# Performance work log

Hardware: AMD Instinct MI355X
Metric: run time of the kernel (lower is better)

## Reference

```python
import jax, jax.numpy as jnp
import numpy as np

N_NODES = 10000
N_EDGES = 160000
HIDDEN = 512
N_LAYERS = 5


def setup_inputs() -> dict:
    key = jax.random.key(0)
    ks = jax.random.split(key, 12)
    return {
        "feat": jax.random.normal(ks[0], (N_NODES, HIDDEN), dtype=jnp.float32),
        "adj_row": jax.random.randint(ks[1], (N_EDGES,), 0, N_NODES, dtype=jnp.int32),
        "adj_col": jax.random.randint(ks[2], (N_EDGES,), 0, N_NODES, dtype=jnp.int32),
        "adj_val": jax.random.uniform(ks[3], (N_EDGES,), dtype=jnp.float32),
        "Wg": jax.random.normal(ks[4], (N_LAYERS, HIDDEN, HIDDEN), dtype=jnp.float32) * 0.02,
        "bg": jnp.zeros((N_LAYERS, HIDDEN), dtype=jnp.float32),
        "vw1": jax.random.normal(ks[5], (HIDDEN, HIDDEN), dtype=jnp.float32) * 0.02,
        "vb1": jnp.zeros((HIDDEN,), dtype=jnp.float32),
        "vw2": jax.random.normal(ks[6], (HIDDEN, 1), dtype=jnp.float32) * 0.02,
        "vb2": jnp.zeros((1,), dtype=jnp.float32),
    }


def _spmm(adj_row, adj_col, adj_val, x, n):
    # out[r] = sum_e adj_val[e] * x[adj_col[e]] for edges with adj_row[e] == r
    gathered = adj_val[:, None] * x[adj_col]  # [E, H]
    return jax.ops.segment_sum(gathered, adj_row, num_segments=n)


def reference(feat, adj_row, adj_col, adj_val, Wg, bg, vw1, vb1, vw2, vb2):
    n = feat.shape[0]
    x = feat
    for i in range(N_LAYERS):  # 5 structurally identical GraphConv layers
        h = x @ Wg[i]                                 # dense GEMM [N,H]
        agg = _spmm(adj_row, adj_col, adj_val, h, n)  # sparse aggregation
        x = jax.nn.relu(agg + bg[i])                  # bias + ReLU (dropout = eval identity)
    h = jax.nn.relu(x @ vw1 + vb1)
    return jax.nn.sigmoid(h @ vw2 + vb2)  # [N, 1]
```

## Files before the change

### kernel.cpp

```cpp
#include <hip/hip_runtime.h>

#define H 512
#define NNODES 10000
#define NEDGES 160000
#define NLAYERS 5

typedef __attribute__((ext_vector_type(8))) short short8;
typedef __attribute__((ext_vector_type(4))) float floatx4;

__device__ inline unsigned short f2bf(float v) {
    union { float f; unsigned int u; } x; x.f = v;
    unsigned int r = (x.u + 0x7fffu + ((x.u >> 16) & 1u)) >> 16;
    return (unsigned short)r;
}
__device__ inline float bf2f(unsigned short u) {
    union { unsigned int u; float f; } x; x.u = ((unsigned int)u) << 16; return x.f;
}
__device__ inline void gl_lds16(const void* g, void* l) {
    __builtin_amdgcn_global_load_lds((const __attribute__((address_space(1))) void*)g,
                                     (__attribute__((address_space(3))) void*)l, 16, 0, 0);
}

__global__ void zero_int(int* __restrict__ p, int n) {
    int i = blockIdx.x * blockDim.x + threadIdx.x;
    if (i < n) p[i] = 0;
}

__global__ void cvt_f32_bf16(const float* __restrict__ in, unsigned short* __restrict__ out, int n4) {
    int i = blockIdx.x * blockDim.x + threadIdx.x;
    if (i < n4) {
        float4 v = ((const float4*)in)[i];
        ushort4 o;
        o.x = f2bf(v.x); o.y = f2bf(v.y); o.z = f2bf(v.z); o.w = f2bf(v.w);
        ((ushort4*)out)[i] = o;
    }
}

__global__ void transpose_cvt6(const float* __restrict__ Wg, const float* __restrict__ vw1,
                               unsigned short* __restrict__ Wt) {
    __shared__ float tile[32][33];
    const int z = blockIdx.z;
    const float* in = (z < NLAYERS) ? (Wg + (size_t)z * H * H) : vw1;
    unsigned short* out = Wt + (size_t)z * H * H;
    const int bx = blockIdx.x * 32;
    const int by = blockIdx.y * 32;
    const int tx = threadIdx.x, ty = threadIdx.y;
    for (int i = ty; i < 32; i += 8)
        tile[i][tx] = in[(size_t)(by + i) * H + bx + tx];
    __syncthreads();
    for (int i = ty; i < 32; i += 8)
        out[(size_t)(bx + i) * H + by + tx] = f2bf(tile[tx][i]);
}

__global__ void edge_hist(const int* __restrict__ rows, int* __restrict__ counts, int n) {
    int i = blockIdx.x * blockDim.x + threadIdx.x;
    if (i < n) atomicAdd(&counts[rows[i]], 1);
}

__global__ __launch_bounds__(1024)
void scan_rows_pad(const int* __restrict__ counts, int* __restrict__ row_ptr, int n) {
    __shared__ int sums[1024];
    const int t = threadIdx.x;
    const int base = t * 16;
    int local[16];
    int s = 0;
#pragma unroll
    for (int i = 0; i < 16; ++i) {
        int idx = base + i;
        int v = (idx < n) ? ((counts[idx] + 7) & ~7) : 0;
        local[i] = s;
        s += v;
    }
    sums[t] = s;
    __syncthreads();
    for (int off = 1; off < 1024; off <<= 1) {
        int v = (t >= off) ? sums[t - off] : 0;
        __syncthreads();
        sums[t] += v;
        __syncthreads();
    }
    const int prefix = (t == 0) ? 0 : sums[t - 1];
#pragma unroll
    for (int i = 0; i < 16; ++i) {
        int idx = base + i;
        if (idx < n) row_ptr[idx] = prefix + local[i];
    }
    if (t == 0) row_ptr[n] = sums[1023];
}

__global__ void edge_scatter(const int* __restrict__ rows, const int* __restrict__ colsin,
                             const float* __restrict__ valsin, const int* __restrict__ row_ptr,
                             int* __restrict__ fill, int* __restrict__ colsout,
                             float* __restrict__ valsout, int n) {
    int i = blockIdx.x * blockDim.x + threadIdx.x;
    if (i < n) {
        int r = rows[i];
        int pos = row_ptr[r] + atomicAdd(&fill[r], 1);
        colsout[pos] = colsin[i];
        valsout[pos] = valsin[i];
    }
}

__device__ __forceinline__ void gemm_tile_body(
    const unsigned short* __restrict__ A, const unsigned short* __restrict__ Bt,
    unsigned short* __restrict__ C, const float* __restrict__ bias,
    int has_bias_relu, int M, int tileM, int tileN,
    unsigned short* lsA, unsigned short* lsB) {
    const int t = threadIdx.x;
    const int lane = t & 63;
    const int wave = t >> 6;
    const int wm = wave >> 1, wn = wave & 1;
    const int quad = lane >> 4, r16 = lane & 15;

    floatx4 acc[4][2] = {};

    const unsigned short* ap[4];
#pragma unroll
    for (int q = 0; q < 4; ++q) {
        const int c = t + 256 * q;
        const int row = c >> 3;
        int g = tileM + row; if (g >= M) g = M - 1;
        ap[q] = A + (size_t)g * 512 + (((c & 7) ^ (row & 7)) * 8);
    }
    const unsigned short* bp[2];
#pragma unroll
    for (int q = 0; q < 2; ++q) {
        const int c = t + 256 * q;
        const int row = c >> 3;
        bp[q] = Bt + (size_t)(tileN + row) * 512 + (((c & 7) ^ (row & 7)) * 8);
    }

    for (int k0 = 0; k0 < 512; k0 += 64) {
        gl_lds16(ap[0] + k0, lsA + (size_t)t * 8);
        gl_lds16(ap[1] + k0, lsA + (size_t)(t + 256) * 8);
        gl_lds16(ap[2] + k0, lsA + (size_t)(t + 512) * 8);
        gl_lds16(ap[3] + k0, lsA + (size_t)(t + 768) * 8);
        gl_lds16(bp[0] + k0, lsB + (size_t)t * 8);
        gl_lds16(bp[1] + k0, lsB + (size_t)(t + 256) * 8);
        __syncthreads();

        short8 af[4][2], bfr[2][2];
#pragma unroll
        for (int i = 0; i < 4; ++i) {
            const int row = wm * 64 + i * 16 + r16;
#pragma unroll
            for (int kk = 0; kk < 2; ++kk) {
                const int kcw = kk * 4 + quad;
                af[i][kk] = *(const short8*)&lsA[(size_t)(row * 8 + (kcw ^ (row & 7))) * 8];
            }
        }
#pragma unroll
        for (int j = 0; j < 2; ++j) {
            const int row = wn * 32 + j * 16 + r16;
#pragma unroll
            for (int kk = 0; kk < 2; ++kk) {
                const int kcw = kk * 4 + quad;
                bfr[j][kk] = *(const short8*)&lsB[(size_t)(row * 8 + (kcw ^ (row & 7))) * 8];
            }
        }
#pragma unroll
        for (int kk = 0; kk < 2; ++kk)
#pragma unroll
            for (int i = 0; i < 4; ++i)
#pragma unroll
                for (int j = 0; j < 2; ++j)
                    acc[i][j] = __builtin_amdgcn_mfma_f32_16x16x32_bf16(af[i][kk], bfr[j][kk], acc[i][j], 0, 0, 0);
        __syncthreads();
    }

#pragma unroll
    for (int i = 0; i < 4; ++i) {
#pragma unroll
        for (int j = 0; j < 2; ++j) {
            const int col = tileN + wn * 32 + j * 16 + r16;
#pragma unroll
            for (int reg = 0; reg < 4; ++reg) {
                const int row = tileM + wm * 64 + i * 16 + quad * 4 + reg;
                if (row < M) {
                    float v = acc[i][j][reg];
                    if (has_bias_relu) { v += bias[col]; v = fmaxf(v, 0.f); }
                    C[(size_t)row * 512 + col] = f2bf(v);
                }
            }
        }
    }
}

__global__ __launch_bounds__(256)
void gemm_bf16_xcd(const unsigned short* __restrict__ A, const unsigned short* __restrict__ Bt,
                   unsigned short* __restrict__ C, const float* __restrict__ bias,
                   int has_bias_relu, int M) {
    __shared__ __align__(16) unsigned short lsA[128 * 64];
    __shared__ __align__(16) unsigned short lsB[64 * 64];
    const int L = blockIdx.x;
    const int m_low = L & 7;
    const int rest = L >> 3;
    const int n = rest & 7;
    const int m_high = rest >> 3;
    const int m = m_high * 8 + m_low;
    gemm_tile_body(A, Bt, C, bias, has_bias_relu, M, m * 128, n * 64, lsA, lsB);
}

__global__ __launch_bounds__(256)
void spmm_pad(const int* __restrict__ prow, const int* __restrict__ cols,
              const float* __restrict__ vals, const unsigned short* __restrict__ hmat,
              const float* __restrict__ bias, unsigned short* __restrict__ xout) {
    const int wave = threadIdx.x >> 6, lane = threadIdx.x & 63;
    const int r = blockIdx.x * 4 + wave;
    if (r >= NNODES) return;
    const int s = prow[r], e = prow[r + 1];
    const int cb = lane * 8;
    float acc[8] = {0.f, 0.f, 0.f, 0.f, 0.f, 0.f, 0.f, 0.f};

    for (int i = s; i < e; i += 8) {
        int c[8]; float v[8]; short8 g[8];
#pragma unroll
        for (int u = 0; u < 8; ++u) { c[u] = cols[i + u]; v[u] = vals[i + u]; }
#pragma unroll
        for (int u = 0; u < 8; ++u) g[u] = *(const short8*)(hmat + (size_t)c[u] * H + cb);
#pragma unroll
        for (int u = 0; u < 8; ++u)
#pragma unroll
            for (int j = 0; j < 8; ++j) acc[j] += v[u] * bf2f((unsigned short)g[u][j]);
    }

    short8 o;
#pragma unroll
    for (int j = 0; j < 8; ++j)
        o[j] = (short)f2bf(fmaxf(acc[j] + bias[cb + j], 0.f));
    *(short8*)(xout + (size_t)r * H + cb) = o;
}

__global__ __launch_bounds__(256)
void final_head(const unsigned short* __restrict__ h2, const float* __restrict__ w2,
                const float* __restrict__ b2, float* __restrict__ out, int n) {
    const int wave = threadIdx.x >> 6, lane = threadIdx.x & 63;
    const int r = blockIdx.x * 4 + wave;
    if (r >= n) return;
    const unsigned short* hrow = h2 + (size_t)r * H;
    float acc = 0.f;
#pragma unroll
    for (int i = 0; i < 8; ++i) {
        const int c = lane * 8 + i;
        acc += bf2f(hrow[c]) * w2[c];
    }
#pragma unroll
    for (int off = 32; off >= 1; off >>= 1) acc += __shfl_xor(acc, off, 64);
    if (lane == 0) out[r] = 1.f / (1.f + expf(-(acc + b2[0])));
}

extern "C" void kernel_launch(void* const* d_in, const int* in_sizes, int n_in,
                              void* d_out, int out_size, void* d_ws, size_t ws_size,
                              hipStream_t stream) {
    (void)in_sizes; (void)n_in; (void)out_size; (void)ws_size;
    const float* feat   = (const float*)d_in[0];
    const int* adj_row  = (const int*)d_in[1];
    const int* adj_col  = (const int*)d_in[2];
    const float* adj_val= (const float*)d_in[3];
    const float* Wg     = (const float*)d_in[4];
    const float* bg     = (const float*)d_in[5];
    const float* vw1    = (const float*)d_in[6];
    const float* vb1    = (const float*)d_in[7];
    const float* vw2    = (const float*)d_in[8];
    const float* vb2    = (const float*)d_in[9];
    float* out = (float*)d_out;

    char* ws = (char*)d_ws;
    unsigned short* x  = (unsigned short*)(ws + 0);
    unsigned short* h  = (unsigned short*)(ws + 10240000);
    unsigned short* Wt = (unsigned short*)(ws + 20480000);
    int*   prow    = (int*)(ws + 23625728);
    int*   counts  = (int*)(ws + 23785792);
    int*   fill    = (int*)(ws + 23825792);
    int*   colsP   = (int*)(ws + 23865792);
    float* valsP   = (float*)(ws + 24825792);

    zero_int<<<(20000 + 255) / 256, 256, 0, stream>>>(counts, 20000);
    zero_int<<<(480000 + 255) / 256, 256, 0, stream>>>(colsP, 480000);
    cvt_f32_bf16<<<(NNODES * H / 4 + 255) / 256, 256, 0, stream>>>(feat, x, NNODES * H / 4);
    transpose_cvt6<<<dim3(16, 16, 6), dim3(32, 8), 0, stream>>>(Wg, vw1, Wt);
    edge_hist<<<(NEDGES + 255) / 256, 256, 0, stream>>>(adj_row, counts, NEDGES);
    scan_rows_pad<<<1, 1024, 0, stream>>>(counts, prow, NNODES);
    edge_scatter<<<(NEDGES + 255) / 256, 256, 0, stream>>>(adj_row, adj_col, adj_val,
                                                           prow, fill, colsP, valsP, NEDGES);

    for (int l = 0; l < NLAYERS; ++l) {
        gemm_bf16_xcd<<<640, 256, 0, stream>>>(x, Wt + (size_t)l * H * H, h, nullptr, 0, NNODES);
        spmm_pad<<<(NNODES + 3) / 4, 256, 0, stream>>>(prow, colsP, valsP, h, bg + (size_t)l * H, x);
    }
    gemm_bf16_xcd<<<640, 256, 0, stream>>>(x, Wt + (size_t)NLAYERS * H * H, h, vb1, 1, NNODES);
    final_head<<<(NNODES + 3) / 4, 256, 0, stream>>>(h, vw2, vb2, out, NNODES);
}
```

Measured before the change: 325.3 us.

## Fuse prep kernels into one launch and enlarge GEMM M-tile to 160 rows

Four setup kernels (the zeroing kernels, the feature conversion and the weight transpose) are merged into a single launch that dispatches on block-index ranges, removing launch overhead. The GEMM M-tile grows from 128 to 160 rows, so the grid becomes 512 blocks (63 M-tiles × 8 N-tiles, with a few idle blocks) and matches the 256 CUs in two waves. The larger tile raises accumulator and LDS use per block, which may reduce occupancy.

```diff
diff --git a/kernel.cpp b/kernel.cpp
--- a/kernel.cpp
+++ b/kernel.cpp
@@ -4,6 +4,8 @@
 #define NNODES 10000
 #define NEDGES 160000
 #define NLAYERS 5
+#define TM 160
+#define NMT 63
 
 typedef __attribute__((ext_vector_type(8))) short short8;
 typedef __attribute__((ext_vector_type(4))) float floatx4;
@@ -21,35 +23,47 @@
                                      (__attribute__((address_space(3))) void*)l, 16, 0, 0);
 }
 
-__global__ void zero_int(int* __restrict__ p, int n) {
-    int i = blockIdx.x * blockDim.x + threadIdx.x;
-    if (i < n) p[i] = 0;
-}
-
-__global__ void cvt_f32_bf16(const float* __restrict__ in, unsigned short* __restrict__ out, int n4) {
-    int i = blockIdx.x * blockDim.x + threadIdx.x;
-    if (i < n4) {
-        float4 v = ((const float4*)in)[i];
-        ushort4 o;
-        o.x = f2bf(v.x); o.y = f2bf(v.y); o.z = f2bf(v.z); o.w = f2bf(v.w);
-        ((ushort4*)out)[i] = o;
-    }
-}
-
-__global__ void transpose_cvt6(const float* __restrict__ Wg, const float* __restrict__ vw1,
-                               unsigned short* __restrict__ Wt) {
-    __shared__ float tile[32][33];
-    const int z = blockIdx.z;
-    const float* in = (z < NLAYERS) ? (Wg + (size_t)z * H * H) : vw1;
-    unsigned short* out = Wt + (size_t)z * H * H;
-    const int bx = blockIdx.x * 32;
-    const int by = blockIdx.y * 32;
-    const int tx = threadIdx.x, ty = threadIdx.y;
-    for (int i = ty; i < 32; i += 8)
-        tile[i][tx] = in[(size_t)(by + i) * H + bx + tx];
-    __syncthreads();
-    for (int i = ty; i < 32; i += 8)
-        out[(size_t)(bx + i) * H + by + tx] = f2bf(tile[tx][i]);
+#define PB_ZERO1 79
+#define PB_ZERO2 1875
+#define PB_CVT   5000
+#define PB_TR    1536
+__global__ __launch_bounds__(256)
+void fused_prep(int* __restrict__ counts, int* __restrict__ colsP,
+                const float* __restrict__ feat, unsigned short* __restrict__ x,
+                const float* __restrict__ Wg, const float* __restrict__ vw1,
+                unsigned short* __restrict__ Wt) {
+    const int b = blockIdx.x;
+    const int t = threadIdx.x;
+    if (b < PB_ZERO1) {
+        int i = b * 256 + t;
+        if (i < 20000) counts[i] = 0;
+    } else if (b < PB_ZERO1 + PB_ZERO2) {
+        int i = (b - PB_ZERO1) * 256 + t;
+        if (i < 480000) colsP[i] = 0;
+    } else if (b < PB_ZERO1 + PB_ZERO2 + PB_CVT) {
+        int i = (b - PB_ZERO1 - PB_ZERO2) * 256 + t;
+        if (i < NNODES * H / 4) {
+            float4 v = ((const float4*)feat)[i];
+            ushort4 o;
+            o.x = f2bf(v.x); o.y = f2bf(v.y); o.z = f2bf(v.z); o.w = f2bf(v.w);
+            ((ushort4*)x)[i] = o;
+        }
+    } else {
+        __shared__ float tile[32][33];
+        const int bb = b - PB_ZERO1 - PB_ZERO2 - PB_CVT;
+        const int z = bb >> 8;
+        const int rem = bb & 255;
+        const int bx = (rem & 15) * 32;
+        const int by = (rem >> 4) * 32;
+        const float* in = (z < NLAYERS) ? (Wg + (size_t)z * H * H) : vw1;
+        unsigned short* out = Wt + (size_t)z * H * H;
+        const int tx = t & 31, ty = t >> 5;
+        for (int i = ty; i < 32; i += 8)
+            tile[i][tx] = in[(size_t)(by + i) * H + bx + tx];
+        __syncthreads();
+        for (int i = ty; i < 32; i += 8)
+            out[(size_t)(bx + i) * H + by + tx] = f2bf(tile[tx][i]);
+    }
 }
 
 __global__ void edge_hist(const int* __restrict__ rows, int* __restrict__ counts, int n) {
@@ -101,22 +115,33 @@
     }
 }
 
-__device__ __forceinline__ void gemm_tile_body(
-    const unsigned short* __restrict__ A, const unsigned short* __restrict__ Bt,
-    unsigned short* __restrict__ C, const float* __restrict__ bias,
-    int has_bias_relu, int M, int tileM, int tileN,
-    unsigned short* lsA, unsigned short* lsB) {
+__global__ __launch_bounds__(256)
+void gemm_bf16_160(const unsigned short* __restrict__ A, const unsigned short* __restrict__ Bt,
+                   unsigned short* __restrict__ C, const float* __restrict__ bias,
+                   int has_bias_relu, int M) {
+    __shared__ __align__(16) unsigned short lsA[TM * 64];
+    __shared__ __align__(16) unsigned short lsB[64 * 64];
+    const int L = blockIdx.x;
+    const int ml = L & 7;
+    const int rest = L >> 3;
+    const int n = rest & 7;
+    const int mh = rest >> 3;
+    const int m = mh * 8 + ml;
+    if (m >= NMT) return;
+    const int tileM = m * TM;
+    const int tileN = n * 64;
+
     const int t = threadIdx.x;
     const int lane = t & 63;
     const int wave = t >> 6;
     const int wm = wave >> 1, wn = wave & 1;
     const int quad = lane >> 4, r16 = lane & 15;
 
-    floatx4 acc[4][2] = {};
-
-    const unsigned short* ap[4];
-#pragma unroll
-    for (int q = 0; q < 4; ++q) {
+    floatx4 acc[5][2] = {};
+
+    const unsigned short* ap[5];
+#pragma unroll
+    for (int q = 0; q < 5; ++q) {
         const int c = t + 256 * q;
         const int row = c >> 3;
         int g = tileM + row; if (g >= M) g = M - 1;
@@ -131,18 +156,17 @@
     }
 
     for (int k0 = 0; k0 < 512; k0 += 64) {
-        gl_lds16(ap[0] + k0, lsA + (size_t)t * 8);
-        gl_lds16(ap[1] + k0, lsA + (size_t)(t + 256) * 8);
-        gl_lds16(ap[2] + k0, lsA + (size_t)(t + 512) * 8);
-        gl_lds16(ap[3] + k0, lsA + (size_t)(t + 768) * 8);
+#pragma unroll
+        for (int q = 0; q < 5; ++q)
+            gl_lds16(ap[q] + k0, lsA + (size_t)(t + 256 * q) * 8);
         gl_lds16(bp[0] + k0, lsB + (size_t)t * 8);
         gl_lds16(bp[1] + k0, lsB + (size_t)(t + 256) * 8);
         __syncthreads();
 
-        short8 af[4][2], bfr[2][2];
-#pragma unroll
-        for (int i = 0; i < 4; ++i) {
-            const int row = wm * 64 + i * 16 + r16;
+        short8 af[5][2], bfr[2][2];
+#pragma unroll
+        for (int i = 0; i < 5; ++i) {
+            const int row = wm * 80 + i * 16 + r16;
 #pragma unroll
             for (int kk = 0; kk < 2; ++kk) {
                 const int kcw = kk * 4 + quad;
@@ -161,7 +185,7 @@
 #pragma unroll
         for (int kk = 0; kk < 2; ++kk)
 #pragma unroll
-            for (int i = 0; i < 4; ++i)
+            for (int i = 0; i < 5; ++i)
 #pragma unroll
                 for (int j = 0; j < 2; ++j)
                     acc[i][j] = __builtin_amdgcn_mfma_f32_16x16x32_bf16(af[i][kk], bfr[j][kk], acc[i][j], 0, 0, 0);
@@ -169,13 +193,13 @@
     }
 
 #pragma unroll
-    for (int i = 0; i < 4; ++i) {
+    for (int i = 0; i < 5; ++i) {
 #pragma unroll
         for (int j = 0; j < 2; ++j) {
             const int col = tileN + wn * 32 + j * 16 + r16;
 #pragma unroll
             for (int reg = 0; reg < 4; ++reg) {
-                const int row = tileM + wm * 64 + i * 16 + quad * 4 + reg;
+                const int row = tileM + wm * 80 + i * 16 + quad * 4 + reg;
                 if (row < M) {
                     float v = acc[i][j][reg];
                     if (has_bias_relu) { v += bias[col]; v = fmaxf(v, 0.f); }
@@ -184,21 +208,6 @@
             }
         }
     }
-}
-
-__global__ __launch_bounds__(256)
-void gemm_bf16_xcd(const unsigned short* __restrict__ A, const unsigned short* __restrict__ Bt,
-                   unsigned short* __restrict__ C, const float* __restrict__ bias,
-                   int has_bias_relu, int M) {
-    __shared__ __align__(16) unsigned short lsA[128 * 64];
-    __shared__ __align__(16) unsigned short lsB[64 * 64];
-    const int L = blockIdx.x;
-    const int m_low = L & 7;
-    const int rest = L >> 3;
-    const int n = rest & 7;
-    const int m_high = rest >> 3;
-    const int m = m_high * 8 + m_low;
-    gemm_tile_body(A, Bt, C, bias, has_bias_relu, M, m * 128, n * 64, lsA, lsB);
 }
 
 __global__ __launch_bounds__(256)
@@ -275,19 +284,17 @@
     int*   colsP   = (int*)(ws + 23865792);
     float* valsP   = (float*)(ws + 24825792);
 
-    zero_int<<<(20000 + 255) / 256, 256, 0, stream>>>(counts, 20000);
-    zero_int<<<(480000 + 255) / 256, 256, 0, stream>>>(colsP, 480000);
-    cvt_f32_bf16<<<(NNODES * H / 4 + 255) / 256, 256, 0, stream>>>(feat, x, NNODES * H / 4);
-    transpose_cvt6<<<dim3(16, 16, 6), dim3(32, 8), 0, stream>>>(Wg, vw1, Wt);
+    fused_prep<<<PB_ZERO1 + PB_ZERO2 + PB_CVT + PB_TR, 256, 0, stream>>>(
+        counts, colsP, feat, x, Wg, vw1, Wt);
     edge_hist<<<(NEDGES + 255) / 256, 256, 0, stream>>>(adj_row, counts, NEDGES);
     scan_rows_pad<<<1, 1024, 0, stream>>>(counts, prow, NNODES);
     edge_scatter<<<(NEDGES + 255) / 256, 256, 0, stream>>>(adj_row, adj_col, adj_val,
                                                            prow, fill, colsP, valsP, NEDGES);
 
     for (int l = 0; l < NLAYERS; ++l) {
-        gemm_bf16_xcd<<<640, 256, 0, stream>>>(x, Wt + (size_t)l * H * H, h, nullptr, 0, NNODES);
+        gemm_bf16_160<<<512, 256, 0, stream>>>(x, Wt + (size_t)l * H * H, h, nullptr, 0, NNODES);
         spmm_pad<<<(NNODES + 3) / 4, 256, 0, stream>>>(prow, colsP, valsP, h, bg + (size_t)l * H, x);
     }
-    gemm_bf16_xcd<<<640, 256, 0, stream>>>(x, Wt + (size_t)NLAYERS * H * H, h, vb1, 1, NNODES);
+    gemm_bf16_160<<<512, 256, 0, stream>>>(x, Wt + (size_t)NLAYERS * H * H, h, vb1, 1, NNODES);
     final_head<<<(NNODES + 3) / 4, 256, 0, stream>>>(h, vw2, vb2, out, NNODES);
 }
```

After: 328.0 us. No clear change (+0.8%).
